# Kernel tuning notes

Hardware: AMD Instinct MI355X
Metric: run time of the kernel (lower is better)

The kernel has to match this reference:

```python
import jax, jax.numpy as jnp
import numpy as np

H, D = 4, 64          # num_heads, hidden_dim
NL, NP, B = 40000, 40000, 64
E_LL, E_LP, E_PL = 160000, 240000, 240000
NEG_SLOPE = 0.2


def _gat(x_src, x_dst, src, dst, Ws, Wd, al, ar, bias, n_dst):
    """DGL GATConv: fc -> edge score -> segment softmax over dst -> scatter-add."""
    fs = (x_src @ Ws).reshape(-1, H, D)            # [Ns,H,D]
    fd = (x_dst @ Wd).reshape(-1, H, D)            # [Nd,H,D]
    el = jnp.sum(fs * al, axis=-1)                 # [Ns,H]
    er = jnp.sum(fd * ar, axis=-1)                 # [Nd,H]
    e = jax.nn.leaky_relu(el[src] + er[dst], NEG_SLOPE)   # [E,H]
    m = jax.lax.stop_gradient(jax.ops.segment_max(e, dst, num_segments=n_dst))
    ex = jnp.exp(e - m[dst])
    s = jax.ops.segment_sum(ex, dst, num_segments=n_dst)
    a = ex / s[dst]                                # edge softmax over in-neighborhoods
    out = jax.ops.segment_sum(fs[src] * a[:, :, None], dst, num_segments=n_dst)
    return out + bias.reshape(1, H, D)


def _gmean(h, gid, nseg):
    s = jax.ops.segment_sum(h, gid, num_segments=nseg)
    c = jax.ops.segment_sum(jnp.ones((h.shape[0], 1), h.dtype), gid, num_segments=nseg)
    return s / jnp.maximum(c, 1.0)


_PARAM_SHAPES = [('W1_ll', (74, 256)), ('al1_ll', (H, D)), ('ar1_ll', (H, D)), ('b1_ll', (256,)),
                 ('W1_lps', (74, 256)), ('W1_lpd', (128, 256)), ('al1_lp', (H, D)), ('ar1_lp', (H, D)), ('b1_lp', (256,)),
                 ('W1_pls', (128, 256)), ('W1_pld', (74, 256)), ('al1_pl', (H, D)), ('ar1_pl', (H, D)), ('b1_pl', (256,)),
                 ('W2_ll', (256, 256)), ('al2_ll', (H, D)), ('ar2_ll', (H, D)), ('b2_ll', (256,)),
                 ('W2_lps', (256, 256)), ('W2_lpd', (256, 256)), ('al2_lp', (H, D)), ('ar2_lp', (H, D)), ('b2_lp', (256,)),
                 ('W2_pls', (256, 256)), ('W2_pld', (256, 256)), ('al2_pl', (H, D)), ('ar2_pl', (H, D)), ('b2_pl', (256,)),
                 ('W_mlp', (512, 256)), ('b_mlp', (256,))]


def setup_inputs() -> dict:
    key = jax.random.key(0)
    ks = iter(jax.random.split(key, 64))
    inp = {}
    inp['x_lig'] = jax.random.normal(next(ks), (NL, 74), jnp.float32)
    inp['x_pro'] = jax.random.normal(next(ks), (NP, 128), jnp.float32)
    for name, shape in _PARAM_SHAPES:
        inp[name] = jax.random.normal(next(ks), shape, jnp.float32) * 0.1
    inp['src_ll'] = jax.random.randint(next(ks), (E_LL,), 0, NL)
    inp['dst_ll'] = jax.random.randint(next(ks), (E_LL,), 0, NL)
    inp['src_lp'] = jax.random.randint(next(ks), (E_LP,), 0, NL)
    inp['dst_lp'] = jax.random.randint(next(ks), (E_LP,), 0, NP)
    inp['src_pl'] = jax.random.randint(next(ks), (E_PL,), 0, NP)
    inp['dst_pl'] = jax.random.randint(next(ks), (E_PL,), 0, NL)
    inp['gid_lig'] = jax.random.randint(next(ks), (NL,), 0, B)
    inp['gid_pro'] = jax.random.randint(next(ks), (NP,), 0, B)
    return inp


def reference(x_lig, x_pro, W1_ll, al1_ll, ar1_ll, b1_ll, W1_lps, W1_lpd, al1_lp, ar1_lp, b1_lp,
              W1_pls, W1_pld, al1_pl, ar1_pl, b1_pl, W2_ll, al2_ll, ar2_ll, b2_ll,
              W2_lps, W2_lpd, al2_lp, ar2_lp, b2_lp, W2_pls, W2_pld, al2_pl, ar2_pl, b2_pl,
              W_mlp, b_mlp, src_ll, dst_ll, src_lp, dst_lp, src_pl, dst_pl, gid_lig, gid_pro):
    # HeteroGraphConv layer 1 (aggregate='sum' over relations per dst ntype)
    h_l = (_gat(x_lig, x_lig, src_ll, dst_ll, W1_ll, W1_ll, al1_ll, ar1_ll, b1_ll, NL)
           + _gat(x_pro, x_lig, src_pl, dst_pl, W1_pls, W1_pld, al1_pl, ar1_pl, b1_pl, NL))
    h_p = _gat(x_lig, x_pro, src_lp, dst_lp, W1_lps, W1_lpd, al1_lp, ar1_lp, b1_lp, NP)
    h_l = jax.nn.relu(h_l.reshape(NL, H * D))
    h_p = jax.nn.relu(h_p.reshape(NP, H * D))
    # HeteroGraphConv layer 2
    h_l2 = (_gat(h_l, h_l, src_ll, dst_ll, W2_ll, W2_ll, al2_ll, ar2_ll, b2_ll, NL)
            + _gat(h_p, h_l, src_pl, dst_pl, W2_pls, W2_pld, al2_pl, ar2_pl, b2_pl, NL))
    h_p2 = _gat(h_l, h_p, src_lp, dst_lp, W2_lps, W2_lpd, al2_lp, ar2_lp, b2_lp, NP)
    h_l2 = jax.nn.relu(h_l2.reshape(NL, H * D))
    h_p2 = jax.nn.relu(h_p2.reshape(NP, H * D))
    # per-graph mean readout (dgl.mean_nodes) + concat + MLP (dropout=eval identity)
    g = jnp.concatenate([_gmean(h_l2, gid_lig, B), _gmean(h_p2, gid_pro, B)], axis=1)  # [B,512]
    return jax.nn.relu(g @ W_mlp + b_mlp)
```

## Files before the change

### kernel.cpp

```cpp
#include <hip/hip_runtime.h>
#include <hip/hip_bf16.h>

#define NLIG 40000
#define NPRO 40000
#define NGRAPH 64
#define ELL 160000
#define ELP 240000
#define EPL 240000

#define RD_STRIPES 256

typedef __hip_bfloat16 bf16;
typedef __attribute__((ext_vector_type(8))) short short8;
typedef __attribute__((ext_vector_type(4))) short short4v;
typedef __attribute__((ext_vector_type(4))) float f32x4;

__device__ __forceinline__ float bits2f(short s) {
  const unsigned u = ((unsigned)(unsigned short)s) << 16;
  return __uint_as_float(u);
}

__global__ __launch_bounds__(256) void convA_kernel(
    const float* __restrict__ A, bf16* __restrict__ hi, bf16* __restrict__ lo,
    int M, int K, int Kp) {
  const int row = blockIdx.x * 8 + (threadIdx.x >> 5);
  if (row >= M) return;
  const int Kp4 = Kp >> 2;
  short* hp = (short*)hi;
  short* lq = (short*)lo;
  for (int c4 = threadIdx.x & 31; c4 < Kp4; c4 += 32) {
    const int k = c4 << 2;
    float v[4];
#pragma unroll
    for (int j = 0; j < 4; ++j) {
      const int kk = k + j;
      v[j] = (kk < K) ? A[(size_t)row * K + kk] : 0.f;
    }
    short4v hv, lv;
#pragma unroll
    for (int j = 0; j < 4; ++j) {
      bf16 h = __float2bfloat16(v[j]);
      float r = v[j] - __bfloat162float(h);
      bf16 l = __float2bfloat16(r);
      hv[j] = *reinterpret_cast<short*>(&h);
      lv[j] = *reinterpret_cast<short*>(&l);
    }
    *reinterpret_cast<short4v*>(&hp[(size_t)row * Kp + k]) = hv;
    *reinterpret_cast<short4v*>(&lq[(size_t)row * Kp + k]) = lv;
  }
}

__global__ __launch_bounds__(256) void convBt_kernel(
    const float* __restrict__ B, bf16* __restrict__ thi, bf16* __restrict__ tlo,
    int K, int Kp) {
  const int tot = 256 * Kp;
  for (int i = blockIdx.x * 256 + threadIdx.x; i < tot; i += gridDim.x * 256) {
    const int n = i / Kp, k = i % Kp;
    float v = (k < K) ? B[(size_t)k * 256 + n] : 0.f;
    bf16 h = __float2bfloat16(v);
    float r = v - __bfloat162float(h);
    thi[i] = h;
    tlo[i] = __float2bfloat16(r);
  }
}

#define LP 40
__global__ __launch_bounds__(256) void mfma_gemm(
    const bf16* __restrict__ AhiP, const bf16* __restrict__ AloP,
    const bf16* __restrict__ BthiP, const bf16* __restrict__ BtloP,
    bf16* __restrict__ C, int M, int Kp,
    const float* __restrict__ al, float* __restrict__ el,
    const float* __restrict__ ar, float* __restrict__ er) {
  __shared__ short sA[2][128 * LP];
  __shared__ short sB[2][128 * LP];
  const short* Ahi = (const short*)AhiP;
  const short* Alo = (const short*)AloP;
  const short* Bthi = (const short*)BthiP;
  const short* Btlo = (const short*)BtloP;
  const int t = threadIdx.x;
  const int w = t >> 6, l = t & 63;
  const int m0 = blockIdx.x * 128;
  const int n0 = blockIdx.y * 128;
  const f32x4 zf = {0.f, 0.f, 0.f, 0.f};
  const short8 zs = {0, 0, 0, 0, 0, 0, 0, 0};
  f32x4 acc[2][8];
#pragma unroll
  for (int i = 0; i < 2; ++i)
#pragma unroll
    for (int j = 0; j < 8; ++j) acc[i][j] = zf;

  const int fr = l & 15, kg = l >> 4;

  for (int k0 = 0; k0 < Kp; k0 += 32) {
#pragma unroll
    for (int rep = 0; rep < 2; ++rep) {
      const int p = t + rep * 256;
      const int row = p >> 2, c = p & 3;
      const int gr = m0 + row;
      short8 vh = zs, vl = zs;
      if (gr < M) {
        const size_t g = (size_t)gr * Kp + k0 + c * 8;
        vh = *(const short8*)(Ahi + g);
        vl = *(const short8*)(Alo + g);
      }
      *(short8*)(&sA[0][row * LP + c * 8]) = vh;
      *(short8*)(&sA[1][row * LP + c * 8]) = vl;
    }
#pragma unroll
    for (int rep = 0; rep < 2; ++rep) {
      const int p = t + rep * 256;
      const int row = p >> 2, c = p & 3;
      const size_t g = (size_t)(n0 + row) * Kp + k0 + c * 8;
      *(short8*)(&sB[0][row * LP + c * 8]) = *(const short8*)(Bthi + g);
      *(short8*)(&sB[1][row * LP + c * 8]) = *(const short8*)(Btlo + g);
    }
    __syncthreads();
    short8 aF[2][2];
#pragma unroll
    for (int i = 0; i < 2; ++i) {
      const int r = (w * 32 + i * 16 + fr) * LP + kg * 8;
      aF[0][i] = *(const short8*)(&sA[0][r]);
      aF[1][i] = *(const short8*)(&sA[1][r]);
    }
#pragma unroll
    for (int j = 0; j < 8; ++j) {
      const int r = (j * 16 + fr) * LP + kg * 8;
      const short8 b0 = *(const short8*)(&sB[0][r]);
      const short8 b1 = *(const short8*)(&sB[1][r]);
#pragma unroll
      for (int i = 0; i < 2; ++i) {
        acc[i][j] = __builtin_amdgcn_mfma_f32_16x16x32_bf16(aF[0][i], b0, acc[i][j], 0, 0, 0);
        acc[i][j] = __builtin_amdgcn_mfma_f32_16x16x32_bf16(aF[0][i], b1, acc[i][j], 0, 0, 0);
        acc[i][j] = __builtin_amdgcn_mfma_f32_16x16x32_bf16(aF[1][i], b0, acc[i][j], 0, 0, 0);
      }
    }
    __syncthreads();
  }

#pragma unroll
  for (int i = 0; i < 2; ++i) {
    const int rbase = m0 + w * 32 + i * 16 + kg * 4;
#pragma unroll
    for (int j = 0; j < 8; ++j) {
      const int col = n0 + j * 16 + fr;
#pragma unroll
      for (int r = 0; r < 4; ++r) {
        const int row = rbase + r;
        if (row < M) C[(size_t)row * 256 + col] = __float2bfloat16(acc[i][j][r]);
      }
    }
  }

  if (el) {
    float alv[8], arv[8];
#pragma unroll
    for (int j = 0; j < 8; ++j) {
      alv[j] = al[n0 + j * 16 + fr];
      arv[j] = er ? ar[n0 + j * 16 + fr] : 0.f;
    }
    const int hb = n0 >> 6;
#pragma unroll
    for (int i = 0; i < 2; ++i) {
#pragma unroll
      for (int r = 0; r < 4; ++r) {
        float sl0 = 0.f, sl1 = 0.f, sr0 = 0.f, sr1 = 0.f;
#pragma unroll
        for (int j = 0; j < 4; ++j) {
          sl0 = fmaf(acc[i][j][r], alv[j], sl0);
          sr0 = fmaf(acc[i][j][r], arv[j], sr0);
          sl1 = fmaf(acc[i][j + 4][r], alv[j + 4], sl1);
          sr1 = fmaf(acc[i][j + 4][r], arv[j + 4], sr1);
        }
        sl0 += __shfl_xor(sl0, 1); sl0 += __shfl_xor(sl0, 2);
        sl0 += __shfl_xor(sl0, 4); sl0 += __shfl_xor(sl0, 8);
        sl1 += __shfl_xor(sl1, 1); sl1 += __shfl_xor(sl1, 2);
        sl1 += __shfl_xor(sl1, 4); sl1 += __shfl_xor(sl1, 8);
        sr0 += __shfl_xor(sr0, 1); sr0 += __shfl_xor(sr0, 2);
        sr0 += __shfl_xor(sr0, 4); sr0 += __shfl_xor(sr0, 8);
        sr1 += __shfl_xor(sr1, 1); sr1 += __shfl_xor(sr1, 2);
        sr1 += __shfl_xor(sr1, 4); sr1 += __shfl_xor(sr1, 8);
        const int row = m0 + w * 32 + i * 16 + kg * 4 + r;
        if (fr == 0 && row < M) {
          el[row * 4 + hb] = sl0;
          el[row * 4 + hb + 1] = sl1;
          if (er) {
            er[row * 4 + hb] = sr0;
            er[row * 4 + hb + 1] = sr1;
          }
        }
      }
    }
  }
}

__global__ void make_wr_kernel(const float* __restrict__ Wd,
                               const float* __restrict__ ar,
                               float* __restrict__ wr, int K) {
  const int t = blockIdx.x * blockDim.x + threadIdx.x;
  if (t < K * 4) {
    const int k = t >> 2, h = t & 3;
    float s = 0.f;
    for (int d = 0; d < 64; ++d)
      s = fmaf(Wd[(size_t)k * 256 + h * 64 + d], ar[h * 64 + d], s);
    wr[t] = s;
  }
}

__global__ __launch_bounds__(256) void er_gemv_kernel(
    const float* __restrict__ X, const float* __restrict__ wr,
    float* __restrict__ er, int n, int K) {
  __shared__ float swr[1024];
  const int t = threadIdx.x;
  for (int i = t; i < K * 4; i += blockDim.x) swr[i] = wr[i];
  __syncthreads();
  const int lane = t & 63;
  const int gw = (blockIdx.x * blockDim.x + t) >> 6;
  if (gw >= n) return;
  float a0 = 0.f, a1 = 0.f, a2 = 0.f, a3 = 0.f;
  for (int k = lane; k < K; k += 64) {
    const float x = X[(size_t)gw * K + k];
    a0 = fmaf(x, swr[k * 4 + 0], a0);
    a1 = fmaf(x, swr[k * 4 + 1], a1);
    a2 = fmaf(x, swr[k * 4 + 2], a2);
    a3 = fmaf(x, swr[k * 4 + 3], a3);
  }
#pragma unroll
  for (int o = 32; o; o >>= 1) {
    a0 += __shfl_xor(a0, o);
    a1 += __shfl_xor(a1, o);
    a2 += __shfl_xor(a2, o);
    a3 += __shfl_xor(a3, o);
  }
  if (lane == 0) {
    er[gw * 4 + 0] = a0; er[gw * 4 + 1] = a1;
    er[gw * 4 + 2] = a2; er[gw * 4 + 3] = a3;
  }
}

__global__ void count_kernel(const int* __restrict__ dst, int* __restrict__ cnt, int E) {
  for (int i = blockIdx.x * blockDim.x + threadIdx.x; i < E; i += gridDim.x * blockDim.x)
    atomicAdd(&cnt[dst[i]], 1);
}

__global__ __launch_bounds__(256) void scan_reduce_kernel(
    const int* __restrict__ data, int* __restrict__ bsum, int n) {
  const int base = blockIdx.x * 1024;
  int s = 0;
  for (int i = threadIdx.x; i < 1024; i += 256) {
    const int idx = base + i;
    s += (idx < n) ? data[idx] : 0;
  }
#pragma unroll
  for (int o = 32; o; o >>= 1) s += __shfl_xor(s, o);
  __shared__ int ws[4];
  if ((threadIdx.x & 63) == 0) ws[threadIdx.x >> 6] = s;
  __syncthreads();
  if (threadIdx.x == 0) bsum[blockIdx.x] = ws[0] + ws[1] + ws[2] + ws[3];
}

__global__ __launch_bounds__(1024) void scan_blocksums_kernel(
    int* __restrict__ bsum, int nb) {
  __shared__ int sm[1024];
  const int t = threadIdx.x;
  const int v = (t < nb) ? bsum[t] : 0;
  sm[t] = v;
  __syncthreads();
  for (int ofs = 1; ofs < 1024; ofs <<= 1) {
    const int tmp = (t >= ofs) ? sm[t - ofs] : 0;
    __syncthreads();
    sm[t] += tmp;
    __syncthreads();
  }
  if (t < nb) bsum[t] = sm[t] - v;
}

__global__ __launch_bounds__(1024) void scan_final_kernel(
    int* __restrict__ data, const int* __restrict__ bsum, int n) {
  __shared__ int sm[1024];
  const int t = threadIdx.x;
  const int i = blockIdx.x * 1024 + t;
  const int v = (i < n) ? data[i] : 0;
  sm[t] = v;
  __syncthreads();
  for (int ofs = 1; ofs < 1024; ofs <<= 1) {
    const int tmp = (t >= ofs) ? sm[t - ofs] : 0;
    __syncthreads();
    sm[t] += tmp;
    __syncthreads();
  }
  const int c = bsum[blockIdx.x];
  if (i < n) data[i] = c + sm[t] - v;
  if (i == n - 1) data[n] = c + sm[t];
}

__global__ void fill_kernel(const int* __restrict__ src, const int* __restrict__ dst,
                            const int* __restrict__ off, int* __restrict__ cursor,
                            int* __restrict__ csrsrc, int E) {
  for (int i = blockIdx.x * blockDim.x + threadIdx.x; i < E; i += gridDim.x * blockDim.x) {
    const int d = dst[i];
    const int p = atomicAdd(&cursor[d], 1);
    csrsrc[off[d] + p] = src[i];
  }
}

__global__ __launch_bounds__(256) void gat_aggregate(
    const bf16* __restrict__ Fb, const float* __restrict__ el,
    const float* __restrict__ er, const int* __restrict__ off,
    const int* __restrict__ csrsrc, float* __restrict__ out,
    int n_dst, int add_flag,
    const float* __restrict__ bias1, const float* __restrict__ bias2, int do_relu) {
  const short* Fp = (const short*)Fb;
  const int lane = threadIdx.x & 63;
  const int myh = lane >> 4;
  const int gw = (blockIdx.x * blockDim.x + threadIdx.x) >> 6;
  if (gw >= n_dst) return;
  const int s0 = off[gw], s1 = off[gw + 1];
  const float ern = er[gw * 4 + myh];
  float4 acc = {0.f, 0.f, 0.f, 0.f};
  float ssum = 0.f;
  for (int p = s0; p < s1; p += 8) {
    const int nb = s1 - p;
    int srcs[8];
#pragma unroll
    for (int b = 0; b < 8; ++b) {
      const int q = (b < nb) ? b : nb - 1;
      srcs[b] = csrsrc[p + q];
    }
    float w8[8];
#pragma unroll
    for (int b = 0; b < 8; ++b) {
      float e = el[srcs[b] * 4 + myh] + ern;
      e = e > 0.f ? e : 0.2f * e;
      w8[b] = (b < nb) ? expf(e) : 0.f;
    }
    short4v f8[8];
#pragma unroll
    for (int b = 0; b < 8; ++b)
      f8[b] = *reinterpret_cast<const short4v*>(&Fp[(size_t)srcs[b] * 256 + lane * 4]);
#pragma unroll
    for (int b = 0; b < 8; ++b) {
      ssum += w8[b];
      acc.x = fmaf(w8[b], bits2f(f8[b][0]), acc.x);
      acc.y = fmaf(w8[b], bits2f(f8[b][1]), acc.y);
      acc.z = fmaf(w8[b], bits2f(f8[b][2]), acc.z);
      acc.w = fmaf(w8[b], bits2f(f8[b][3]), acc.w);
    }
  }
  const float inv = ssum > 0.f ? 1.f / ssum : 0.f;
  float4 res = {acc.x * inv, acc.y * inv, acc.z * inv, acc.w * inv};
  float4* po = reinterpret_cast<float4*>(&out[(size_t)gw * 256 + lane * 4]);
  if (add_flag) {
    const float4 prev = *po;
    res.x += prev.x; res.y += prev.y; res.z += prev.z; res.w += prev.w;
  }
  if (bias1) {
    float4 bb = *reinterpret_cast<const float4*>(&bias1[lane * 4]);
    if (bias2) {
      const float4 b2 = *reinterpret_cast<const float4*>(&bias2[lane * 4]);
      bb.x += b2.x; bb.y += b2.y; bb.z += b2.z; bb.w += b2.w;
    }
    res.x += bb.x; res.y += bb.y; res.z += bb.z; res.w += bb.w;
  }
  if (do_relu) {
    res.x = fmaxf(res.x, 0.f); res.y = fmaxf(res.y, 0.f);
    res.z = fmaxf(res.z, 0.f); res.w = fmaxf(res.w, 0.f);
  }
  *po = res;
}

__global__ __launch_bounds__(256) void graph_sum_v3(
    const float* __restrict__ h, const int* __restrict__ gid,
    float* __restrict__ pbuf, int n) {
  __shared__ float sm[NGRAPH * 256];
  const int t = threadIdx.x;
  for (int i = t; i < NGRAPH * 256; i += 256) sm[i] = 0.f;
  __syncthreads();
  const int chunk = (n + RD_STRIPES - 1) / RD_STRIPES;
  const int lo = blockIdx.x * chunk;
  const int hiN = min(n, lo + chunk);
#pragma unroll 8
  for (int node = lo; node < hiN; ++node) {
    const int g = gid[node];
    const float v = h[(size_t)node * 256 + t];
    sm[g * 256 + t] += v;
  }
  __syncthreads();
  float* dst = pbuf + (size_t)blockIdx.x * (NGRAPH * 256);
  for (int i = t; i < NGRAPH * 256; i += 256) dst[i] = sm[i];
}

__global__ __launch_bounds__(256) void graph_reduce_kernel(
    const float* __restrict__ pbuf, float* __restrict__ gsum, int colofs) {
  const int g = blockIdx.x, t = threadIdx.x;
  float acc = 0.f;
#pragma unroll 8
  for (int s = 0; s < RD_STRIPES; ++s)
    acc += pbuf[(size_t)s * (NGRAPH * 256) + g * 256 + t];
  gsum[(size_t)g * 512 + colofs + t] = acc;
}

__global__ __launch_bounds__(256) void graph_count_kernel(
    const int* __restrict__ gid, int* __restrict__ gcnt, int n, int cntofs) {
  __shared__ int c[NGRAPH];
  if (threadIdx.x < NGRAPH) c[threadIdx.x] = 0;
  __syncthreads();
  for (int i = blockIdx.x * blockDim.x + threadIdx.x; i < n; i += gridDim.x * blockDim.x)
    atomicAdd(&c[gid[i]], 1);
  __syncthreads();
  if (threadIdx.x < NGRAPH && c[threadIdx.x])
    atomicAdd(&gcnt[cntofs + threadIdx.x], c[threadIdx.x]);
}

__global__ __launch_bounds__(256) void mlp_kernel(
    const float* __restrict__ gsum, const int* __restrict__ gcnt,
    const float* __restrict__ Wm, const float* __restrict__ bm,
    float* __restrict__ out) {
  __shared__ float g[512];
  const int b = blockIdx.x, t = threadIdx.x;
  const float cl = fmaxf((float)gcnt[b], 1.f);
  const float cp = fmaxf((float)gcnt[64 + b], 1.f);
  for (int k = t; k < 512; k += 256)
    g[k] = gsum[(size_t)b * 512 + k] * (k < 256 ? 1.f / cl : 1.f / cp);
  __syncthreads();
  float acc = bm[t];
  for (int k = 0; k < 512; ++k) acc = fmaf(g[k], Wm[(size_t)k * 256 + t], acc);
  out[b * 256 + t] = fmaxf(acc, 0.f);
}

extern "C" void kernel_launch(void* const* d_in, const int* in_sizes, int n_in,
                              void* d_out, int out_size, void* d_ws, size_t ws_size,
                              hipStream_t stream) {
  const float* x_lig  = (const float*)d_in[0];
  const float* x_pro  = (const float*)d_in[1];
  const float* W1_ll  = (const float*)d_in[2];
  const float* al1_ll = (const float*)d_in[3];
  const float* ar1_ll = (const float*)d_in[4];
  const float* b1_ll  = (const float*)d_in[5];
  const float* W1_lps = (const float*)d_in[6];
  const float* W1_lpd = (const float*)d_in[7];
  const float* al1_lp = (const float*)d_in[8];
  const float* ar1_lp = (const float*)d_in[9];
  const float* b1_lp  = (const float*)d_in[10];
  const float* W1_pls = (const float*)d_in[11];
  const float* W1_pld = (const float*)d_in[12];
  const float* al1_pl = (const float*)d_in[13];
  const float* ar1_pl = (const float*)d_in[14];
  const float* b1_pl  = (const float*)d_in[15];
  const float* W2_ll  = (const float*)d_in[16];
  const float* al2_ll = (const float*)d_in[17];
  const float* ar2_ll = (const float*)d_in[18];
  const float* b2_ll  = (const float*)d_in[19];
  const float* W2_lps = (const float*)d_in[20];
  const float* W2_lpd = (const float*)d_in[21];
  const float* al2_lp = (const float*)d_in[22];
  const float* ar2_lp = (const float*)d_in[23];
  const float* b2_lp  = (const float*)d_in[24];
  const float* W2_pls = (const float*)d_in[25];
  const float* W2_pld = (const float*)d_in[26];
  const float* al2_pl = (const float*)d_in[27];
  const float* ar2_pl = (const float*)d_in[28];
  const float* b2_pl  = (const float*)d_in[29];
  const float* W_mlp  = (const float*)d_in[30];
  const float* b_mlp  = (const float*)d_in[31];
  const int* src_ll   = (const int*)d_in[32];
  const int* dst_ll   = (const int*)d_in[33];
  const int* src_lp   = (const int*)d_in[34];
  const int* dst_lp   = (const int*)d_in[35];
  const int* src_pl   = (const int*)d_in[36];
  const int* dst_pl   = (const int*)d_in[37];
  const int* gid_lig  = (const int*)d_in[38];
  const int* gid_pro  = (const int*)d_in[39];
  float* out = (float*)d_out;
  (void)in_sizes; (void)n_in; (void)out_size; (void)ws_size;

  size_t cur = 0;
  auto carve = [&](size_t bytes) -> char* {
    char* p = (char*)d_ws + cur;
    cur += (bytes + 511) & ~(size_t)511;
    return p;
  };
  const size_t NB = (size_t)40000 * 256 * sizeof(float);
  bf16* Fb    = (bf16*)carve(NB);
  float* h_l  = (float*)carve(NB);
  float* h_p  = (float*)carve(NB);
  float* hX   = (float*)carve(NB);
  char*  S    = carve(NB);
  float* el   = (float*)carve((size_t)40000 * 4 * sizeof(float));
  float* er   = (float*)carve((size_t)40000 * 4 * sizeof(float));
  float* erPL = (float*)carve((size_t)40000 * 4 * sizeof(float));
  float* erLP = (float*)carve((size_t)40000 * 4 * sizeof(float));
  float* wr   = (float*)carve((size_t)256 * 4 * sizeof(float));
  bf16* Bthi  = (bf16*)carve((size_t)256 * 256 * sizeof(bf16));
  bf16* Btlo  = (bf16*)carve((size_t)256 * 256 * sizeof(bf16));
  float* gsum = (float*)carve((size_t)64 * 512 * sizeof(float));
  int* gcnt   = (int*)carve(128 * sizeof(int));
  int* bsum   = (int*)carve(1025 * sizeof(int));
  int* off_ll = (int*)carve((NLIG + 1) * sizeof(int));
  int* off_lp = (int*)carve((NPRO + 1) * sizeof(int));
  int* off_pl = (int*)carve((NLIG + 1) * sizeof(int));
  int* cursor = (int*)carve((NLIG + 1) * sizeof(int));
  int* csr_ll = (int*)carve((size_t)ELL * sizeof(int));
  int* csr_lp = (int*)carve((size_t)ELP * sizeof(int));
  int* csr_pl = (int*)carve((size_t)EPL * sizeof(int));

  bf16* XLhi = (bf16*)S;
  bf16* XLlo = XLhi + (size_t)40000 * 96;
  bf16* XPhi = XLlo + (size_t)40000 * 96;
  bf16* XPlo = XPhi + (size_t)40000 * 128;
  bf16* S1hi = (bf16*)S;
  bf16* S1lo = S1hi + (size_t)40000 * 256;
  float* P2  = (float*)S;
  bf16* S2hi = (bf16*)h_l;
  bf16* S2lo = S2hi + (size_t)40000 * 256;
  float* pbuf = (float*)Fb;

  const int B256 = 256;
  auto thrGrid  = [](long long n) { return (int)((n + 255) / 256); };
  auto waveGrid = [](int n) { return (n + 3) / 4; };

  auto conv_a = [&](const float* A, bf16* hi, bf16* lo, int M, int K, int Kp) {
    convA_kernel<<<(M + 7) / 8, B256, 0, stream>>>(A, hi, lo, M, K, Kp);
  };
  auto run_mfma = [&](const bf16* ahi, const bf16* alo, const float* W, int K, int Kp,
                      bf16* C, int M, const float* alv, float* elp,
                      const float* arv, float* erp) {
    convBt_kernel<<<256, B256, 0, stream>>>(W, Bthi, Btlo, K, Kp);
    dim3 g((M + 127) / 128, 2);
    mfma_gemm<<<g, B256, 0, stream>>>(ahi, alo, Bthi, Btlo, C, M, Kp, alv, elp, arv, erp);
  };
  auto run_er_gemv = [&](const float* Wd, const float* arv, const float* X,
                         float* dst_er, int n, int K) {
    make_wr_kernel<<<(K * 4 + 255) / 256, B256, 0, stream>>>(Wd, arv, wr, K);
    er_gemv_kernel<<<waveGrid(n), B256, 0, stream>>>(X, wr, dst_er, n, K);
  };
  auto run_agg = [&](const int* off, const int* csr, int nDst, float* outbuf, int addf,
                     const float* erp, const float* bias1, const float* bias2, int relu) {
    gat_aggregate<<<waveGrid(nDst), B256, 0, stream>>>(
        Fb, el, erp, off, csr, outbuf, nDst, addf, bias1, bias2, relu);
  };
  auto run_scan = [&](int* data, int n) {
    const int nb = (n + 1023) / 1024;
    scan_reduce_kernel<<<nb, B256, 0, stream>>>(data, bsum, n);
    scan_blocksums_kernel<<<1, 1024, 0, stream>>>(bsum, nb);
    scan_final_kernel<<<nb, 1024, 0, stream>>>(data, bsum, n);
  };

  struct Rel { const int* src; const int* dst; int* off; int* csr; int E; int Nd; };
  Rel rels[3] = {
    {src_ll, dst_ll, off_ll, csr_ll, ELL, NLIG},
    {src_lp, dst_lp, off_lp, csr_lp, ELP, NPRO},
    {src_pl, dst_pl, off_pl, csr_pl, EPL, NLIG},
  };
  for (int r = 0; r < 3; ++r) {
    hipMemsetAsync(rels[r].off, 0, (rels[r].Nd + 1) * sizeof(int), stream);
    count_kernel<<<thrGrid(rels[r].E), B256, 0, stream>>>(rels[r].dst, rels[r].off, rels[r].E);
    run_scan(rels[r].off, rels[r].Nd);
    hipMemsetAsync(cursor, 0, (rels[r].Nd + 1) * sizeof(int), stream);
    fill_kernel<<<thrGrid(rels[r].E), B256, 0, stream>>>(
        rels[r].src, rels[r].dst, rels[r].off, cursor, rels[r].csr, rels[r].E);
  }

  conv_a(x_lig, XLhi, XLlo, NLIG, 74, 96);
  conv_a(x_pro, XPhi, XPlo, NPRO, 128, 128);
  run_mfma(XLhi, XLlo, W1_ll, 74, 96, Fb, NLIG, al1_ll, el, ar1_ll, er);
  run_agg(off_ll, csr_ll, NLIG, h_l, 0, er, nullptr, nullptr, 0);
  run_er_gemv(W1_pld, ar1_pl, x_lig, er, NLIG, 74);
  run_mfma(XPhi, XPlo, W1_pls, 128, 128, Fb, NPRO, al1_pl, el, nullptr, nullptr);
  run_agg(off_pl, csr_pl, NLIG, h_l, 1, er, b1_ll, b1_pl, 1);
  run_er_gemv(W1_lpd, ar1_lp, x_pro, er, NPRO, 128);
  run_mfma(XLhi, XLlo, W1_lps, 74, 96, Fb, NLIG, al1_lp, el, nullptr, nullptr);
  run_agg(off_lp, csr_lp, NPRO, h_p, 0, er, b1_lp, nullptr, 1);

  run_er_gemv(W2_pld, ar2_pl, h_l, erPL, NLIG, 256);
  run_er_gemv(W2_lpd, ar2_lp, h_p, erLP, NPRO, 256);
  conv_a(h_l, S1hi, S1lo, NLIG, 256, 256);
  run_mfma(S1hi, S1lo, W2_ll, 256, 256, Fb, NLIG, al2_ll, el, ar2_ll, er);
  run_agg(off_ll, csr_ll, NLIG, hX, 0, er, nullptr, nullptr, 0);
  run_mfma(S1hi, S1lo, W2_lps, 256, 256, Fb, NLIG, al2_lp, el, nullptr, nullptr);
  run_agg(off_lp, csr_lp, NPRO, P2, 0, erLP, b2_lp, nullptr, 1);
  conv_a(h_p, S2hi, S2lo, NPRO, 256, 256);
  run_mfma(S2hi, S2lo, W2_pls, 256, 256, Fb, NPRO, al2_pl, el, nullptr, nullptr);
  run_agg(off_pl, csr_pl, NLIG, hX, 1, erPL, b2_ll, b2_pl, 1);

  hipMemsetAsync(gcnt, 0, 128 * sizeof(int), stream);
  graph_sum_v3<<<RD_STRIPES, B256, 0, stream>>>(hX, gid_lig, pbuf, NLIG);
  graph_reduce_kernel<<<NGRAPH, B256, 0, stream>>>(pbuf, gsum, 0);
  graph_count_kernel<<<64, B256, 0, stream>>>(gid_lig, gcnt, NLIG, 0);
  graph_sum_v3<<<RD_STRIPES, B256, 0, stream>>>(P2, gid_pro, pbuf, NPRO);
  graph_reduce_kernel<<<NGRAPH, B256, 0, stream>>>(pbuf, gsum, 256);
  graph_count_kernel<<<64, B256, 0, stream>>>(gid_pro, gcnt, NPRO, 64);
  mlp_kernel<<<64, B256, 0, stream>>>(gsum, gcnt, W_mlp, b_mlp, out);
}
```

Before: 693.7 us.

## Fuse both relation aggregations per destination and emit bf16 split plus er in epilogue

Replaces the per-relation aggregate kernel with a fused one that walks both incoming relations for a destination node in a single pass. It adds bias and ReLU, then writes either fp32 output or the hi/lo bf16 split consumed by the next GEMM, and computes the layer-2 er projection with a wave reduction. This removes the read-modify-write of partial outputs, the separate conv_a split passes and the layer-2 er_gemv launches. The cost is double-buffered feature and score buffers, more workspace, and an extra conv_a of x_lig because its buffer is reused.

```diff
diff --git a/kernel.cpp b/kernel.cpp
--- a/kernel.cpp
+++ b/kernel.cpp
@@ -303,19 +303,9 @@
   }
 }
 
-__global__ __launch_bounds__(256) void gat_aggregate(
-    const bf16* __restrict__ Fb, const float* __restrict__ el,
-    const float* __restrict__ er, const int* __restrict__ off,
-    const int* __restrict__ csrsrc, float* __restrict__ out,
-    int n_dst, int add_flag,
-    const float* __restrict__ bias1, const float* __restrict__ bias2, int do_relu) {
-  const short* Fp = (const short*)Fb;
-  const int lane = threadIdx.x & 63;
-  const int myh = lane >> 4;
-  const int gw = (blockIdx.x * blockDim.x + threadIdx.x) >> 6;
-  if (gw >= n_dst) return;
-  const int s0 = off[gw], s1 = off[gw + 1];
-  const float ern = er[gw * 4 + myh];
+__device__ __forceinline__ float4 agg_walk(
+    const short* __restrict__ Fp, const float* __restrict__ el, float ern,
+    const int* __restrict__ csr, int s0, int s1, int myh, int lane) {
   float4 acc = {0.f, 0.f, 0.f, 0.f};
   float ssum = 0.f;
   for (int p = s0; p < s1; p += 8) {
@@ -324,7 +314,7 @@
 #pragma unroll
     for (int b = 0; b < 8; ++b) {
       const int q = (b < nb) ? b : nb - 1;
-      srcs[b] = csrsrc[p + q];
+      srcs[b] = csr[p + q];
     }
     float w8[8];
 #pragma unroll
@@ -347,25 +337,81 @@
     }
   }
   const float inv = ssum > 0.f ? 1.f / ssum : 0.f;
-  float4 res = {acc.x * inv, acc.y * inv, acc.z * inv, acc.w * inv};
-  float4* po = reinterpret_cast<float4*>(&out[(size_t)gw * 256 + lane * 4]);
-  if (add_flag) {
-    const float4 prev = *po;
-    res.x += prev.x; res.y += prev.y; res.z += prev.z; res.w += prev.w;
-  }
-  if (bias1) {
+  float4 r = {acc.x * inv, acc.y * inv, acc.z * inv, acc.w * inv};
+  return r;
+}
+
+__global__ __launch_bounds__(256) void gat_agg_fused(
+    const bf16* __restrict__ F1, const float* __restrict__ el1,
+    const float* __restrict__ er1, const int* __restrict__ off1,
+    const int* __restrict__ csr1,
+    const bf16* __restrict__ F2, const float* __restrict__ el2,
+    const float* __restrict__ er2, const int* __restrict__ off2,
+    const int* __restrict__ csr2,
+    const float* __restrict__ bias1, const float* __restrict__ bias2,
+    float* __restrict__ outF, bf16* __restrict__ outHi, bf16* __restrict__ outLo,
+    const float* __restrict__ wr2, float* __restrict__ erOut,
+    int n_dst) {
+  const int lane = threadIdx.x & 63;
+  const int myh = lane >> 4;
+  const int gw = (blockIdx.x * blockDim.x + threadIdx.x) >> 6;
+  if (gw >= n_dst) return;
+
+  float4 res = agg_walk((const short*)F1, el1, er1[gw * 4 + myh],
+                        csr1, off1[gw], off1[gw + 1], myh, lane);
+  if (F2) {
+    const float4 r2 = agg_walk((const short*)F2, el2, er2[gw * 4 + myh],
+                               csr2, off2[gw], off2[gw + 1], myh, lane);
+    res.x += r2.x; res.y += r2.y; res.z += r2.z; res.w += r2.w;
+  }
+  {
     float4 bb = *reinterpret_cast<const float4*>(&bias1[lane * 4]);
     if (bias2) {
       const float4 b2 = *reinterpret_cast<const float4*>(&bias2[lane * 4]);
       bb.x += b2.x; bb.y += b2.y; bb.z += b2.z; bb.w += b2.w;
     }
-    res.x += bb.x; res.y += bb.y; res.z += bb.z; res.w += bb.w;
-  }
-  if (do_relu) {
-    res.x = fmaxf(res.x, 0.f); res.y = fmaxf(res.y, 0.f);
-    res.z = fmaxf(res.z, 0.f); res.w = fmaxf(res.w, 0.f);
-  }
-  *po = res;
+    res.x = fmaxf(res.x + bb.x, 0.f);
+    res.y = fmaxf(res.y + bb.y, 0.f);
+    res.z = fmaxf(res.z + bb.z, 0.f);
+    res.w = fmaxf(res.w + bb.w, 0.f);
+  }
+  if (outF) {
+    *reinterpret_cast<float4*>(&outF[(size_t)gw * 256 + lane * 4]) = res;
+  } else {
+    const float rv[4] = {res.x, res.y, res.z, res.w};
+    short4v hv, lv;
+#pragma unroll
+    for (int j = 0; j < 4; ++j) {
+      bf16 h = __float2bfloat16(rv[j]);
+      float r = rv[j] - __bfloat162float(h);
+      bf16 l = __float2bfloat16(r);
+      hv[j] = *reinterpret_cast<const short*>(&h);
+      lv[j] = *reinterpret_cast<const short*>(&l);
+    }
+    *reinterpret_cast<short4v*>(&((short*)outHi)[(size_t)gw * 256 + lane * 4]) = hv;
+    *reinterpret_cast<short4v*>(&((short*)outLo)[(size_t)gw * 256 + lane * 4]) = lv;
+  }
+  if (erOut) {
+    float4 wv0 = *reinterpret_cast<const float4*>(&wr2[(lane * 4 + 0) * 4]);
+    float4 wv1 = *reinterpret_cast<const float4*>(&wr2[(lane * 4 + 1) * 4]);
+    float4 wv2 = *reinterpret_cast<const float4*>(&wr2[(lane * 4 + 2) * 4]);
+    float4 wv3 = *reinterpret_cast<const float4*>(&wr2[(lane * 4 + 3) * 4]);
+    float e0 = res.x * wv0.x + res.y * wv1.x + res.z * wv2.x + res.w * wv3.x;
+    float e1 = res.x * wv0.y + res.y * wv1.y + res.z * wv2.y + res.w * wv3.y;
+    float e2 = res.x * wv0.z + res.y * wv1.z + res.z * wv2.z + res.w * wv3.z;
+    float e3 = res.x * wv0.w + res.y * wv1.w + res.z * wv2.w + res.w * wv3.w;
+#pragma unroll
+    for (int o = 32; o; o >>= 1) {
+      e0 += __shfl_xor(e0, o);
+      e1 += __shfl_xor(e1, o);
+      e2 += __shfl_xor(e2, o);
+      e3 += __shfl_xor(e3, o);
+    }
+    if (lane == 0) {
+      erOut[gw * 4 + 0] = e0; erOut[gw * 4 + 1] = e1;
+      erOut[gw * 4 + 2] = e2; erOut[gw * 4 + 3] = e3;
+    }
+  }
 }
 
 __global__ __launch_bounds__(256) void graph_sum_v3(
@@ -479,17 +525,22 @@
     cur += (bytes + 511) & ~(size_t)511;
     return p;
   };
-  const size_t NB = (size_t)40000 * 256 * sizeof(float);
-  bf16* Fb    = (bf16*)carve(NB);
-  float* h_l  = (float*)carve(NB);
-  float* h_p  = (float*)carve(NB);
+  const size_t NB   = (size_t)40000 * 256 * sizeof(float);
+  const size_t NBH  = (size_t)40000 * 256 * sizeof(bf16);
+  bf16* FbA   = (bf16*)carve(NBH);
+  bf16* FbB   = (bf16*)carve(NBH);
+  char* S1    = carve(NB);
+  char* S2P   = carve(NB);
   float* hX   = (float*)carve(NB);
-  char*  S    = carve(NB);
-  float* el   = (float*)carve((size_t)40000 * 4 * sizeof(float));
-  float* er   = (float*)carve((size_t)40000 * 4 * sizeof(float));
+  float* elA  = (float*)carve((size_t)40000 * 4 * sizeof(float));
+  float* erA  = (float*)carve((size_t)40000 * 4 * sizeof(float));
+  float* elB  = (float*)carve((size_t)40000 * 4 * sizeof(float));
+  float* erB  = (float*)carve((size_t)40000 * 4 * sizeof(float));
   float* erPL = (float*)carve((size_t)40000 * 4 * sizeof(float));
   float* erLP = (float*)carve((size_t)40000 * 4 * sizeof(float));
-  float* wr   = (float*)carve((size_t)256 * 4 * sizeof(float));
+  float* wr1  = (float*)carve((size_t)256 * 4 * sizeof(float));
+  float* wrA  = (float*)carve((size_t)256 * 4 * sizeof(float));
+  float* wrB  = (float*)carve((size_t)256 * 4 * sizeof(float));
   bf16* Bthi  = (bf16*)carve((size_t)256 * 256 * sizeof(bf16));
   bf16* Btlo  = (bf16*)carve((size_t)256 * 256 * sizeof(bf16));
   float* gsum = (float*)carve((size_t)64 * 512 * sizeof(float));
@@ -503,16 +554,16 @@
   int* csr_lp = (int*)carve((size_t)ELP * sizeof(int));
   int* csr_pl = (int*)carve((size_t)EPL * sizeof(int));
 
-  bf16* XLhi = (bf16*)S;
+  bf16* XLhi = (bf16*)S1;
   bf16* XLlo = XLhi + (size_t)40000 * 96;
-  bf16* XPhi = XLlo + (size_t)40000 * 96;
+  bf16* XPhi = (bf16*)S2P;
   bf16* XPlo = XPhi + (size_t)40000 * 128;
-  bf16* S1hi = (bf16*)S;
+  bf16* S1hi = (bf16*)S1;
   bf16* S1lo = S1hi + (size_t)40000 * 256;
-  float* P2  = (float*)S;
-  bf16* S2hi = (bf16*)h_l;
+  bf16* S2hi = (bf16*)S2P;
   bf16* S2lo = S2hi + (size_t)40000 * 256;
-  float* pbuf = (float*)Fb;
+  float* P2  = (float*)S2P;
+  float* pbuf = (float*)FbA;
 
   const int B256 = 256;
   auto thrGrid  = [](long long n) { return (int)((n + 255) / 256); };
@@ -527,16 +578,6 @@
     convBt_kernel<<<256, B256, 0, stream>>>(W, Bthi, Btlo, K, Kp);
     dim3 g((M + 127) / 128, 2);
     mfma_gemm<<<g, B256, 0, stream>>>(ahi, alo, Bthi, Btlo, C, M, Kp, alv, elp, arv, erp);
-  };
-  auto run_er_gemv = [&](const float* Wd, const float* arv, const float* X,
-                         float* dst_er, int n, int K) {
-    make_wr_kernel<<<(K * 4 + 255) / 256, B256, 0, stream>>>(Wd, arv, wr, K);
-    er_gemv_kernel<<<waveGrid(n), B256, 0, stream>>>(X, wr, dst_er, n, K);
-  };
-  auto run_agg = [&](const int* off, const int* csr, int nDst, float* outbuf, int addf,
-                     const float* erp, const float* bias1, const float* bias2, int relu) {
-    gat_aggregate<<<waveGrid(nDst), B256, 0, stream>>>(
-        Fb, el, erp, off, csr, outbuf, nDst, addf, bias1, bias2, relu);
   };
   auto run_scan = [&](int* data, int n) {
     const int nb = (n + 1023) / 1024;
@@ -562,25 +603,36 @@
 
   conv_a(x_lig, XLhi, XLlo, NLIG, 74, 96);
   conv_a(x_pro, XPhi, XPlo, NPRO, 128, 128);
-  run_mfma(XLhi, XLlo, W1_ll, 74, 96, Fb, NLIG, al1_ll, el, ar1_ll, er);
-  run_agg(off_ll, csr_ll, NLIG, h_l, 0, er, nullptr, nullptr, 0);
-  run_er_gemv(W1_pld, ar1_pl, x_lig, er, NLIG, 74);
-  run_mfma(XPhi, XPlo, W1_pls, 128, 128, Fb, NPRO, al1_pl, el, nullptr, nullptr);
-  run_agg(off_pl, csr_pl, NLIG, h_l, 1, er, b1_ll, b1_pl, 1);
-  run_er_gemv(W1_lpd, ar1_lp, x_pro, er, NPRO, 128);
-  run_mfma(XLhi, XLlo, W1_lps, 74, 96, Fb, NLIG, al1_lp, el, nullptr, nullptr);
-  run_agg(off_lp, csr_lp, NPRO, h_p, 0, er, b1_lp, nullptr, 1);
-
-  run_er_gemv(W2_pld, ar2_pl, h_l, erPL, NLIG, 256);
-  run_er_gemv(W2_lpd, ar2_lp, h_p, erLP, NPRO, 256);
-  conv_a(h_l, S1hi, S1lo, NLIG, 256, 256);
-  run_mfma(S1hi, S1lo, W2_ll, 256, 256, Fb, NLIG, al2_ll, el, ar2_ll, er);
-  run_agg(off_ll, csr_ll, NLIG, hX, 0, er, nullptr, nullptr, 0);
-  run_mfma(S1hi, S1lo, W2_lps, 256, 256, Fb, NLIG, al2_lp, el, nullptr, nullptr);
-  run_agg(off_lp, csr_lp, NPRO, P2, 0, erLP, b2_lp, nullptr, 1);
-  conv_a(h_p, S2hi, S2lo, NPRO, 256, 256);
-  run_mfma(S2hi, S2lo, W2_pls, 256, 256, Fb, NPRO, al2_pl, el, nullptr, nullptr);
-  run_agg(off_pl, csr_pl, NLIG, hX, 1, erPL, b2_ll, b2_pl, 1);
+  run_mfma(XLhi, XLlo, W1_ll, 74, 96, FbA, NLIG, al1_ll, elA, ar1_ll, erA);
+  run_mfma(XPhi, XPlo, W1_pls, 128, 128, FbB, NPRO, al1_pl, elB, nullptr, nullptr);
+  make_wr_kernel<<<(74 * 4 + 255) / 256, B256, 0, stream>>>(W1_pld, ar1_pl, wr1, 74);
+  er_gemv_kernel<<<waveGrid(NLIG), B256, 0, stream>>>(x_lig, wr1, erB, NLIG, 74);
+  make_wr_kernel<<<(256 * 4 + 255) / 256, B256, 0, stream>>>(W2_pld, ar2_pl, wrA, 256);
+  gat_agg_fused<<<waveGrid(NLIG), B256, 0, stream>>>(
+      FbA, elA, erA, off_ll, csr_ll,
+      FbB, elB, erB, off_pl, csr_pl,
+      b1_ll, b1_pl, nullptr, S1hi, S1lo, wrA, erPL, NLIG);
+  make_wr_kernel<<<(128 * 4 + 255) / 256, B256, 0, stream>>>(W1_lpd, ar1_lp, wr1, 128);
+  er_gemv_kernel<<<waveGrid(NPRO), B256, 0, stream>>>(x_pro, wr1, erB, NPRO, 128);
+  make_wr_kernel<<<(256 * 4 + 255) / 256, B256, 0, stream>>>(W2_lpd, ar2_lp, wrB, 256);
+  conv_a(x_lig, XPhi, XPlo, NLIG, 74, 96);
+  run_mfma(XPhi, XPlo, W1_lps, 74, 96, FbB, NLIG, al1_lp, elB, nullptr, nullptr);
+  gat_agg_fused<<<waveGrid(NPRO), B256, 0, stream>>>(
+      FbB, elB, erB, off_lp, csr_lp,
+      nullptr, nullptr, nullptr, nullptr, nullptr,
+      b1_lp, nullptr, nullptr, S2hi, S2lo, wrB, erLP, NPRO);
+
+  run_mfma(S1hi, S1lo, W2_ll, 256, 256, FbA, NLIG, al2_ll, elA, ar2_ll, erA);
+  run_mfma(S2hi, S2lo, W2_pls, 256, 256, FbB, NPRO, al2_pl, elB, nullptr, nullptr);
+  gat_agg_fused<<<waveGrid(NLIG), B256, 0, stream>>>(
+      FbA, elA, erA, off_ll, csr_ll,
+      FbB, elB, erPL, off_pl, csr_pl,
+      b2_ll, b2_pl, hX, nullptr, nullptr, nullptr, nullptr, NLIG);
+  run_mfma(S1hi, S1lo, W2_lps, 256, 256, FbA, NLIG, al2_lp, elA, nullptr, nullptr);
+  gat_agg_fused<<<waveGrid(NPRO), B256, 0, stream>>>(
+      FbA, elA, erLP, off_lp, csr_lp,
+      nullptr, nullptr, nullptr, nullptr, nullptr,
+      b2_lp, nullptr, P2, nullptr, nullptr, nullptr, nullptr, NPRO);
 
   hipMemsetAsync(gcnt, 0, 128 * sizeof(int), stream);
   graph_sum_v3<<<RD_STRIPES, B256, 0, stream>>>(hX, gid_lig, pbuf, NLIG);
```

Measured after the change: 637.2 us. 1.09x faster.
